# Kernel tuning notes

Hardware: AMD Instinct MI355X
Metric: run time of the kernel (lower is better)

The kernel has to match this reference:

```python
import jax, jax.numpy as jnp
import numpy as np

B, S, D, H = 2, 2048, 1024, 16
HD = D // H


def setup_inputs() -> dict:
    key = jax.random.key(0)
    ks = jax.random.split(key, 9)
    sc = 0.02
    return {
        "x": jax.random.normal(ks[0], (B, S, D), dtype=jnp.float32),
        "qw": jax.random.normal(ks[1], (D, D), dtype=jnp.float32) * sc,
        "qb": jax.random.normal(ks[2], (D,), dtype=jnp.float32) * sc,
        "kw": jax.random.normal(ks[3], (D, D), dtype=jnp.float32) * sc,
        "kb": jax.random.normal(ks[4], (D,), dtype=jnp.float32) * sc,
        "vw": jax.random.normal(ks[5], (D, D), dtype=jnp.float32) * sc,
        "vb": jax.random.normal(ks[6], (D,), dtype=jnp.float32) * sc,
        "ow": jax.random.normal(ks[7], (D, D), dtype=jnp.float32) * sc,
        "ob": jax.random.normal(ks[8], (D,), dtype=jnp.float32) * sc,
    }


def reference(x, qw, qb, kw, kb, vw, vb, ow, ob):
    b, s, d = x.shape
    # projections (torch Linear: x @ W.T + b)
    q = (x @ qw.T + qb).reshape(b, s, H, HD).transpose(0, 2, 1, 3)  # bhsd
    k = (x @ kw.T + kb).reshape(b, s, H, HD).transpose(0, 2, 1, 3)
    v = (x @ vw.T + vb).reshape(b, s, H, HD).transpose(0, 2, 1, 3)
    scale = 1.0 / jnp.sqrt(jnp.float32(HD))
    score = jnp.einsum("bhsd,bhtd->bhst", q, k) * scale  # bhss
    # causal mask: -inf strictly above diagonal
    mask = jnp.triu(jnp.full((s, s), -jnp.inf, dtype=score.dtype), k=1)
    score = jax.nn.softmax(score + mask, axis=-1)
    o = jnp.einsum("bhst,bhtd->bhsd", score, v)
    o = o.transpose(0, 2, 1, 3).reshape(b, s, d)
    return o @ ow.T + ob
```

## Files before the change

kernel.cpp:

```cpp
#include <hip/hip_runtime.h>
#include <hip/hip_bf16.h>
#include <stdint.h>

typedef __bf16 bf16x8 __attribute__((ext_vector_type(8)));
typedef __bf16 bf16x4 __attribute__((ext_vector_type(4)));
typedef float f32x4 __attribute__((ext_vector_type(4)));
typedef unsigned short ushort_t;


__device__ inline ushort_t f2bf(float f) {
  union { float f; uint32_t u; } v; v.f = f;
  uint32_t r = (v.u + 0x7fffu + ((v.u >> 16) & 1u)) >> 16;
  return (ushort_t)r;
}

__device__ inline void gll16(const void* g, void* l) {
  __builtin_amdgcn_global_load_lds((const __attribute__((address_space(1))) void*)g,
                                   (__attribute__((address_space(3))) void*)l, 16, 0, 0);
}

__global__ void cvt_x(const float* __restrict__ in, ushort_t* __restrict__ out) {
  int i = blockIdx.x * blockDim.x + threadIdx.x;
  float4 f = ((const float4*)in)[i];
  union { ushort_t u[4]; uint2 v; } r;
  r.u[0] = f2bf(f.x); r.u[1] = f2bf(f.y); r.u[2] = f2bf(f.z); r.u[3] = f2bf(f.w);
  ((uint2*)out)[i] = r.v;
}
__global__ void cvt_w(const float* __restrict__ a, const float* __restrict__ b,
                      const float* __restrict__ c, const float* __restrict__ d,
                      ushort_t* __restrict__ out) {
  const float* srcs[4] = {a, b, c, d};
  const float* s = srcs[blockIdx.y];
  ushort_t* o = out + (size_t)blockIdx.y * 1048576;
  int i = blockIdx.x * blockDim.x + threadIdx.x;
  float4 f = ((const float4*)s)[i];
  union { ushort_t u[4]; uint2 v; } r;
  r.u[0] = f2bf(f.x); r.u[1] = f2bf(f.y); r.u[2] = f2bf(f.z); r.u[3] = f2bf(f.w);
  ((uint2*)(o))[i] = r.v;
}

#define NKT 16

__device__ inline void stage_half(const ushort_t* __restrict__ g, ushort_t* l, int tid) {
  #pragma unroll
  for (int i = 0; i < 2; i++) {
    int c = tid + i * 512;
    int row = c >> 3;
    int q = (c & 7) ^ (row & 7);
    gll16(g + (size_t)row * 1024 + q * 8, l + c * 8);
  }
}

__global__ __launch_bounds__(512, 2) void qkv_gemm(
    const ushort_t* __restrict__ xb,
    const ushort_t* __restrict__ qwb, const ushort_t* __restrict__ kwb, const ushort_t* __restrict__ vwb,
    const float* __restrict__ qbias, const float* __restrict__ kbias, const float* __restrict__ vbias,
    ushort_t* __restrict__ qo, ushort_t* __restrict__ ko, ushort_t* __restrict__ vto)
{
  const int z = blockIdx.y;
  const int bx = blockIdx.x;
  const float* bias = (z == 0) ? qbias : (z == 1) ? kbias : vbias;
  const ushort_t* Ap;
  const ushort_t* Bp;
  int m0, n0;
  if (z == 2) {
    Ap = vwb; Bp = xb;
    m0 = (bx & 3) * 256;
    n0 = (bx >> 2) * 256;
  } else {
    Ap = xb; Bp = (z == 0) ? qwb : kwb;
    m0 = (bx >> 2) * 256;
    n0 = (bx & 3) * 256;
  }

  __shared__ __align__(16) ushort_t As[2][2][128 * 64];
  __shared__ __align__(16) ushort_t Bs[2][2][128 * 64];

  const int tid = threadIdx.x;
  const int w = tid >> 6;
  const int lane = tid & 63;
  const int ln = lane & 15;
  const int q4 = lane >> 4;
  const int wm = w & 1;
  const int wn = w >> 1;
  const int bh = wn >> 1;
  const int brow0 = (wn & 1) * 64;

  f32x4 acc[8][4];
  #pragma unroll
  for (int i = 0; i < 8; i++)
    #pragma unroll
    for (int j = 0; j < 4; j++) acc[i][j] = f32x4{0.f, 0.f, 0.f, 0.f};

  stage_half(Ap + (size_t)(m0 +   0) * 1024 +  0, &As[0][0][0], tid);
  stage_half(Ap + (size_t)(m0 + 128) * 1024 +  0, &As[0][1][0], tid);
  stage_half(Bp + (size_t)(n0 +   0) * 1024 +  0, &Bs[0][0][0], tid);
  stage_half(Bp + (size_t)(n0 + 128) * 1024 +  0, &Bs[0][1][0], tid);
  stage_half(Bp + (size_t)(n0 +   0) * 1024 + 64, &Bs[1][0][0], tid);
  stage_half(Bp + (size_t)(n0 + 128) * 1024 + 64, &Bs[1][1][0], tid);
  asm volatile("s_waitcnt vmcnt(4)" ::: "memory");
  __builtin_amdgcn_s_barrier();

  const int achk = ln & 7;

  for (int t = 0; t < NKT; ++t) {
    const int buf = t & 1;
    const ushort_t* Abuf = &As[buf][wm][0];
    const ushort_t* Bbuf = &Bs[buf][bh][0];

    bf16x8 a0[4][2], a4[4][2], b0[2][2], b2[2][2];

    #pragma unroll
    for (int m = 0; m < 4; m++)
      #pragma unroll
      for (int ks = 0; ks < 2; ks++)
        a0[m][ks] = *(const bf16x8*)&Abuf[(m * 16 + ln) * 64 + (((ks * 4 + q4) ^ achk) * 8)];
    #pragma unroll
    for (int n = 0; n < 2; n++)
      #pragma unroll
      for (int ks = 0; ks < 2; ks++)
        b0[n][ks] = *(const bf16x8*)&Bbuf[(brow0 + n * 16 + ln) * 64 + (((ks * 4 + q4) ^ achk) * 8)];
    if (t + 1 < NKT)
      stage_half(Ap + (size_t)m0 * 1024 + (t + 1) * 64, &As[(t + 1) & 1][0][0], tid);
    __builtin_amdgcn_s_barrier();
    asm volatile("s_waitcnt lgkmcnt(0)" ::: "memory");
    __builtin_amdgcn_s_setprio(1);
    #pragma unroll
    for (int m = 0; m < 4; m++)
      #pragma unroll
      for (int n = 0; n < 2; n++)
        #pragma unroll
        for (int ks = 0; ks < 2; ks++)
          acc[m][n] = __builtin_amdgcn_mfma_f32_16x16x32_bf16(a0[m][ks], b0[n][ks], acc[m][n], 0, 0, 0);
    __builtin_amdgcn_s_setprio(0);
    __builtin_amdgcn_s_barrier();

    #pragma unroll
    for (int n = 0; n < 2; n++)
      #pragma unroll
      for (int ks = 0; ks < 2; ks++)
        b2[n][ks] = *(const bf16x8*)&Bbuf[(brow0 + (n + 2) * 16 + ln) * 64 + (((ks * 4 + q4) ^ achk) * 8)];
    if (t + 1 < NKT)
      stage_half(Ap + (size_t)(m0 + 128) * 1024 + (t + 1) * 64, &As[(t + 1) & 1][1][0], tid);
    __builtin_amdgcn_s_barrier();
    asm volatile("s_waitcnt lgkmcnt(0)" ::: "memory");
    __builtin_amdgcn_s_setprio(1);
    #pragma unroll
    for (int m = 0; m < 4; m++)
      #pragma unroll
      for (int n = 0; n < 2; n++)
        #pragma unroll
        for (int ks = 0; ks < 2; ks++)
          acc[m][n + 2] = __builtin_amdgcn_mfma_f32_16x16x32_bf16(a0[m][ks], b2[n][ks], acc[m][n + 2], 0, 0, 0);
    __builtin_amdgcn_s_setprio(0);
    __builtin_amdgcn_s_barrier();

    #pragma unroll
    for (int m = 0; m < 4; m++)
      #pragma unroll
      for (int ks = 0; ks < 2; ks++)
        a4[m][ks] = *(const bf16x8*)&Abuf[((m + 4) * 16 + ln) * 64 + (((ks * 4 + q4) ^ achk) * 8)];
    if (t + 2 < NKT)
      stage_half(Bp + (size_t)n0 * 1024 + (t + 2) * 64, &Bs[buf][0][0], tid);
    __builtin_amdgcn_s_barrier();
    asm volatile("s_waitcnt lgkmcnt(0)" ::: "memory");
    __builtin_amdgcn_s_setprio(1);
    #pragma unroll
    for (int m = 0; m < 4; m++)
      #pragma unroll
      for (int n = 0; n < 2; n++)
        #pragma unroll
        for (int ks = 0; ks < 2; ks++)
          acc[m + 4][n + 2] = __builtin_amdgcn_mfma_f32_16x16x32_bf16(a4[m][ks], b2[n][ks], acc[m + 4][n + 2], 0, 0, 0);
    __builtin_amdgcn_s_setprio(0);
    __builtin_amdgcn_s_barrier();

    if (t + 2 < NKT)
      stage_half(Bp + (size_t)(n0 + 128) * 1024 + (t + 2) * 64, &Bs[buf][1][0], tid);
    __builtin_amdgcn_s_barrier();
    __builtin_amdgcn_s_setprio(1);
    #pragma unroll
    for (int m = 0; m < 4; m++)
      #pragma unroll
      for (int n = 0; n < 2; n++)
        #pragma unroll
        for (int ks = 0; ks < 2; ks++)
          acc[m + 4][n] = __builtin_amdgcn_mfma_f32_16x16x32_bf16(a4[m][ks], b0[n][ks], acc[m + 4][n], 0, 0, 0);
    __builtin_amdgcn_s_setprio(0);
    if (t + 2 < NKT) {
      asm volatile("s_waitcnt vmcnt(4)" ::: "memory");
    } else if (t + 1 < NKT) {
      asm volatile("s_waitcnt vmcnt(0)" ::: "memory");
    }
    __builtin_amdgcn_s_barrier();
  }

  if (z == 2) {
    #pragma unroll
    for (int n = 0; n < 4; n++) {
      int col = n0 + wn * 64 + n * 16 + ln;
      int bb = col >> 11, s = col & 2047;
      size_t base = (size_t)bb * 2097152 + s;
      #pragma unroll
      for (int m = 0; m < 8; m++) {
        int prow = m0 + wm * 128 + m * 16 + q4 * 4;
        #pragma unroll
        for (int r = 0; r < 4; r++) {
          int p = prow + r;
          vto[base + (size_t)p * 2048] = f2bf(acc[m][n][r] + bias[p]);
        }
      }
    }
  } else {
    #pragma unroll
    for (int n = 0; n < 4; n++) {
      int col = n0 + wn * 64 + n * 16 + ln;
      float bv = bias[col];
      int h = col >> 6, hd = col & 63;
      #pragma unroll
      for (int m = 0; m < 8; m++) {
        int rowb = m0 + wm * 128 + m * 16 + q4 * 4;
        #pragma unroll
        for (int r = 0; r < 4; r++) {
          int row = rowb + r;
          int b = row >> 11, s = row & 2047;
          float val = acc[m][n][r] + bv;
          if (z == 0) {
            qo[((size_t)((b * 16 + h) * 2048 + s)) * 64 + hd] = f2bf(val * 0.180336884f);
          } else {
            ko[((size_t)((b * 16 + h) * 2048 + s)) * 64 + hd] = f2bf(val);
          }
        }
      }
    }
  }
}

#define PAD 72
#define PPAD 68
__global__ __launch_bounds__(256) void attn(
    const ushort_t* __restrict__ qp, const ushort_t* __restrict__ kp,
    const ushort_t* __restrict__ vtp, ushort_t* __restrict__ op)
{
  __shared__ __align__(16) ushort_t Ks[64 * PAD];
  __shared__ __align__(16) ushort_t Vts[64 * PAD];
  __shared__ __align__(16) ushort_t Ps[4][16 * PPAD];

  const int tid = threadIdx.x;
  const int w = tid >> 6;
  const int lane = tid & 63;
  const int ln = lane & 15;
  const int q4 = lane >> 4;
  const int bh = blockIdx.y;
  const int b = bh >> 4, h = bh & 15;
  int tswz = (blockIdx.x + blockIdx.y) & 31;
  const int qt = (blockIdx.y & 16) ? (31 - tswz) : tswz;
  const int q0 = qt * 64;
  const int nt = qt + 1;

  const int c0 = tid, c1 = tid + 256;
  const int kr0_row = c0 >> 3, kr0_col = (c0 & 7) * 8;
  const int kr1_row = c1 >> 3, kr1_col = (c1 & 7) * 8;

  bf16x8 onesf;
  {
    union { ushort_t u[8]; bf16x8 v; } t;
    #pragma unroll
    for (int j = 0; j < 8; j++) t.u[j] = 0x3F80;
    onesf = t.v;
  }

  bf16x8 qf[2];
  {
    const ushort_t* base = qp + ((size_t)bh * 2048 + q0 + w * 16 + ln) * 64 + q4 * 8;
    qf[0] = *(const bf16x8*)(base);
    qf[1] = *(const bf16x8*)(base + 32);
  }

  f32x4 acc_o[4];
  f32x4 acc_l = f32x4{0.f, 0.f, 0.f, 0.f};
  #pragma unroll
  for (int t = 0; t < 4; t++) acc_o[t] = f32x4{0.f, 0.f, 0.f, 0.f};

  const ushort_t* kb = kp + (size_t)bh * 2048 * 64;
  const ushort_t* vb = vtp + (size_t)bh * 64 * 2048;

  uint4 kr0, kr1, vr0, vr1;
  kr0 = *(const uint4*)(kb + kr0_row * 64 + kr0_col);
  kr1 = *(const uint4*)(kb + kr1_row * 64 + kr1_col);
  vr0 = *(const uint4*)(vb + (size_t)kr0_row * 2048 + kr0_col);
  vr1 = *(const uint4*)(vb + (size_t)kr1_row * 2048 + kr1_col);

  for (int it = 0; it < nt; it++) {
    if (it) __syncthreads();
    *(uint4*)(&Ks [kr0_row * PAD + kr0_col]) = kr0;
    *(uint4*)(&Ks [kr1_row * PAD + kr1_col]) = kr1;
    *(uint4*)(&Vts[kr0_row * PAD + kr0_col]) = vr0;
    *(uint4*)(&Vts[kr1_row * PAD + kr1_col]) = vr1;
    __syncthreads();

    if (it + 1 < nt) {
      int kv1 = (it + 1) * 64;
      kr0 = *(const uint4*)(kb + (size_t)kv1 * 64 + kr0_row * 64 + kr0_col);
      kr1 = *(const uint4*)(kb + (size_t)kv1 * 64 + kr1_row * 64 + kr1_col);
      vr0 = *(const uint4*)(vb + (size_t)kr0_row * 2048 + kv1 + kr0_col);
      vr1 = *(const uint4*)(vb + (size_t)kr1_row * 2048 + kv1 + kr1_col);
    }

    f32x4 sc[4];
    #pragma unroll
    for (int t = 0; t < 4; t++) sc[t] = f32x4{0.f, 0.f, 0.f, 0.f};
    __builtin_amdgcn_s_setprio(1);
    #pragma unroll
    for (int ks = 0; ks < 2; ks++) {
      bf16x8 kf[4];
      #pragma unroll
      for (int tn = 0; tn < 4; tn++)
        kf[tn] = *(const bf16x8*)(&Ks[(tn * 16 + ln) * PAD + ks * 32 + q4 * 8]);
      #pragma unroll
      for (int tn = 0; tn < 4; tn++)
        sc[tn] = __builtin_amdgcn_mfma_f32_16x16x32_bf16(qf[ks], kf[tn], sc[tn], 0, 0, 0);
    }
    __builtin_amdgcn_s_setprio(0);

    if (it == qt) {
      int qrow = w * 16 + q4 * 4;
      #pragma unroll
      for (int tn = 0; tn < 4; tn++) {
        int col = tn * 16 + ln;
        #pragma unroll
        for (int r = 0; r < 4; r++)
          if (col > qrow + r) sc[tn][r] = -__builtin_inff();
      }
    }
    #pragma unroll
    for (int tn = 0; tn < 4; tn++)
      #pragma unroll
      for (int r = 0; r < 4; r++) {
        float p = __builtin_amdgcn_exp2f(sc[tn][r]);
        Ps[w][(q4 * 4 + r) * PPAD + tn * 16 + ln] = (ushort_t)(__float_as_uint(p) >> 16);
      }
    __builtin_amdgcn_s_setprio(1);
    #pragma unroll
    for (int ks = 0; ks < 2; ks++) {
      bf16x8 vf[4];
      #pragma unroll
      for (int tn = 0; tn < 4; tn++)
        vf[tn] = *(const bf16x8*)(&Vts[(tn * 16 + ln) * PAD + ks * 32 + q4 * 8]);
      const ushort_t* pp = &Ps[w][ln * PPAD + ks * 32 + q4 * 8];
      bf16x4 plo = *(const bf16x4*)(pp);
      bf16x4 phi = *(const bf16x4*)(pp + 4);
      bf16x8 pf = __builtin_shufflevector(plo, phi, 0, 1, 2, 3, 4, 5, 6, 7);
      acc_l = __builtin_amdgcn_mfma_f32_16x16x32_bf16(pf, onesf, acc_l, 0, 0, 0);
      #pragma unroll
      for (int tn = 0; tn < 4; tn++)
        acc_o[tn] = __builtin_amdgcn_mfma_f32_16x16x32_bf16(pf, vf[tn], acc_o[tn], 0, 0, 0);
    }
    __builtin_amdgcn_s_setprio(0);
  }

  {
    float invl[4];
    #pragma unroll
    for (int r = 0; r < 4; r++) invl[r] = __builtin_amdgcn_rcpf(acc_l[r]);
    #pragma unroll
    for (int tn = 0; tn < 4; tn++)
      #pragma unroll
      for (int r = 0; r < 4; r++) {
        int row = q0 + w * 16 + q4 * 4 + r;
        op[((size_t)b * 2048 + row) * 1024 + h * 64 + tn * 16 + ln] =
            f2bf(acc_o[tn][r] * invl[r]);
      }
  }
}

__global__ __launch_bounds__(256) void out_gemm(
    const ushort_t* __restrict__ ob_in, const ushort_t* __restrict__ owb,
    const float* __restrict__ obias, float* __restrict__ out)
{
  __shared__ __align__(16) ushort_t As[3][64 * 64];
  __shared__ __align__(16) ushort_t Bs[3][128 * 64];

  const int tid = threadIdx.x;
  const int w = tid >> 6;
  const int lane = tid & 63;
  const int ln = lane & 15;
  const int q4 = lane >> 4;
  const int wm = w & 1, wn = w >> 1;
  const int m0 = blockIdx.y * 64;
  const int n0 = blockIdx.x * 128;

  f32x4 acc[2][4];
  #pragma unroll
  for (int i = 0; i < 2; i++)
    #pragma unroll
    for (int j = 0; j < 4; j++) acc[i][j] = f32x4{0.f, 0.f, 0.f, 0.f};

  auto STAGE = [&](int bi, int k0) {
    #pragma unroll
    for (int i = 0; i < 2; i++) {
      int c = tid + i * 256;
      int row = c >> 3;
      int cq = (c & 7) ^ (row & 7);
      gll16(&ob_in[(size_t)(m0 + row) * 1024 + k0 + cq * 8], &As[bi][c * 8]);
    }
    #pragma unroll
    for (int i = 0; i < 4; i++) {
      int c = tid + i * 256;
      int row = c >> 3;
      int cq = (c & 7) ^ (row & 7);
      gll16(&owb[(size_t)(n0 + row) * 1024 + k0 + cq * 8], &Bs[bi][c * 8]);
    }
  };

  STAGE(0, 0);
  STAGE(1, 64);
  asm volatile("s_waitcnt vmcnt(6)" ::: "memory");
  __builtin_amdgcn_s_barrier();

  #pragma unroll
  for (int t = 0; t < 16; t++) {
    const int cb = t % 3;
    if (t + 2 < 16) STAGE((t + 2) % 3, (t + 2) * 64);
    #pragma unroll
    for (int ks = 0; ks < 2; ks++) {
      bf16x8 af[2], bfr[4];
      #pragma unroll
      for (int tt = 0; tt < 2; tt++) {
        int rr = wm * 32 + tt * 16 + ln;
        af[tt] = *(const bf16x8*)(&As[cb][rr * 64 + (((ks * 4 + q4) ^ (rr & 7)) * 8)]);
      }
      #pragma unroll
      for (int tt = 0; tt < 4; tt++) {
        int rc = wn * 64 + tt * 16 + ln;
        bfr[tt] = *(const bf16x8*)(&Bs[cb][rc * 64 + (((ks * 4 + q4) ^ (rc & 7)) * 8)]);
      }
      #pragma unroll
      for (int tm = 0; tm < 2; tm++)
        #pragma unroll
        for (int tn = 0; tn < 4; tn++)
          acc[tm][tn] = __builtin_amdgcn_mfma_f32_16x16x32_bf16(af[tm], bfr[tn], acc[tm][tn], 0, 0, 0);
    }
    if (t + 2 < 16) {
      asm volatile("s_waitcnt vmcnt(6)" ::: "memory");
    } else if (t + 1 < 16) {
      asm volatile("s_waitcnt vmcnt(0)" ::: "memory");
    }
    __builtin_amdgcn_s_barrier();
  }

  #pragma unroll
  for (int tn = 0; tn < 4; tn++) {
    int col = n0 + wn * 64 + tn * 16 + ln;
    float bv = obias[col];
    #pragma unroll
    for (int tm = 0; tm < 2; tm++) {
      int rowb = m0 + wm * 32 + tm * 16 + q4 * 4;
      #pragma unroll
      for (int r = 0; r < 4; r++)
        out[(size_t)(rowb + r) * 1024 + col] = acc[tm][tn][r] + bv;
    }
  }
}

extern "C" void kernel_launch(void* const* d_in, const int* in_sizes, int n_in,
                              void* d_out, int out_size, void* d_ws, size_t ws_size,
                              hipStream_t stream) {
  const float* x     = (const float*)d_in[0];
  const float* qw    = (const float*)d_in[1];
  const float* qb    = (const float*)d_in[2];
  const float* kw    = (const float*)d_in[3];
  const float* kb    = (const float*)d_in[4];
  const float* vw    = (const float*)d_in[5];
  const float* vb    = (const float*)d_in[6];
  const float* ow    = (const float*)d_in[7];
  const float* obias = (const float*)d_in[8];
  float* out = (float*)d_out;

  char* ws = (char*)d_ws;
  ushort_t* xb  = (ushort_t*)(ws);
  ushort_t* wb  = (ushort_t*)(ws + 8388608);
  ushort_t* qwb = wb;
  ushort_t* kwb = wb + 1048576;
  ushort_t* vwb = wb + 2097152;
  ushort_t* owb = wb + 3145728;
  ushort_t* qo  = (ushort_t*)(ws + 16777216);
  ushort_t* ko  = (ushort_t*)(ws + 25165824);
  ushort_t* vto = (ushort_t*)(ws + 33554432);
  ushort_t* oo  = (ushort_t*)(ws + 41943040);

  cvt_x<<<dim3(4096), dim3(256), 0, stream>>>(x, xb);
  cvt_w<<<dim3(1024, 4), dim3(256), 0, stream>>>(qw, kw, vw, ow, wb);

  qkv_gemm<<<dim3(64, 3), dim3(512), 0, stream>>>(xb, qwb, kwb, vwb, qb, kb, vb, qo, ko, vto);
  attn<<<dim3(32, 32), dim3(256), 0, stream>>>(qo, ko, vto, oo);
  out_gemm<<<dim3(8, 64), dim3(256), 0, stream>>>(oo, owb, obias, out);
}
```

Measured before the change: 193.5 us.

## Double-buffer attention K/V tiles with 128-row query blocks and merge conversion kernels

The attention kernel now processes 128 query rows per block with 8 waves, and K/V tiles are double-buffered in shared memory with loads issued two tiles ahead. This removes one of the two barriers per iteration and lets each K/V tile be reused by twice as many query rows. The x and weight fp32-to-bf16 conversions are merged into a single launch. The cost is more shared memory and registers per block, fewer blocks in the grid, and wasted fully-masked work on the last diagonal tile for the upper waves.

```diff
diff --git a/kernel.cpp b/kernel.cpp
--- a/kernel.cpp
+++ b/kernel.cpp
@@ -19,24 +19,28 @@
                                    (__attribute__((address_space(3))) void*)l, 16, 0, 0);
 }
 
-__global__ void cvt_x(const float* __restrict__ in, ushort_t* __restrict__ out) {
-  int i = blockIdx.x * blockDim.x + threadIdx.x;
-  float4 f = ((const float4*)in)[i];
-  union { ushort_t u[4]; uint2 v; } r;
-  r.u[0] = f2bf(f.x); r.u[1] = f2bf(f.y); r.u[2] = f2bf(f.z); r.u[3] = f2bf(f.w);
-  ((uint2*)out)[i] = r.v;
-}
-__global__ void cvt_w(const float* __restrict__ a, const float* __restrict__ b,
-                      const float* __restrict__ c, const float* __restrict__ d,
-                      ushort_t* __restrict__ out) {
-  const float* srcs[4] = {a, b, c, d};
-  const float* s = srcs[blockIdx.y];
-  ushort_t* o = out + (size_t)blockIdx.y * 1048576;
-  int i = blockIdx.x * blockDim.x + threadIdx.x;
+__global__ void cvt_all(const float* __restrict__ x,
+                        const float* __restrict__ qw, const float* __restrict__ kw,
+                        const float* __restrict__ vw, const float* __restrict__ ow,
+                        ushort_t* __restrict__ xb, ushort_t* __restrict__ wb) {
+  int bid = blockIdx.x;
+  const float* s;
+  ushort_t* o;
+  int i;
+  if (bid < 4096) {
+    s = x; o = xb; i = bid * 256 + threadIdx.x;
+  } else {
+    int j = bid - 4096;
+    int wi = j >> 10;
+    const float* srcs[4] = {qw, kw, vw, ow};
+    s = srcs[wi];
+    o = wb + (size_t)wi * 1048576;
+    i = (j & 1023) * 256 + threadIdx.x;
+  }
   float4 f = ((const float4*)s)[i];
   union { ushort_t u[4]; uint2 v; } r;
   r.u[0] = f2bf(f.x); r.u[1] = f2bf(f.y); r.u[2] = f2bf(f.z); r.u[3] = f2bf(f.w);
-  ((uint2*)(o))[i] = r.v;
+  ((uint2*)o)[i] = r.v;
 }
 
 #define NKT 16
@@ -238,13 +242,13 @@
 
 #define PAD 72
 #define PPAD 68
-__global__ __launch_bounds__(256) void attn(
+__global__ __launch_bounds__(512) void attn(
     const ushort_t* __restrict__ qp, const ushort_t* __restrict__ kp,
     const ushort_t* __restrict__ vtp, ushort_t* __restrict__ op)
 {
-  __shared__ __align__(16) ushort_t Ks[64 * PAD];
-  __shared__ __align__(16) ushort_t Vts[64 * PAD];
-  __shared__ __align__(16) ushort_t Ps[4][16 * PPAD];
+  __shared__ __align__(16) ushort_t Ks[2][64 * PAD];
+  __shared__ __align__(16) ushort_t Vts[2][64 * PAD];
+  __shared__ __align__(16) ushort_t Ps[8][16 * PPAD];
 
   const int tid = threadIdx.x;
   const int w = tid >> 6;
@@ -253,14 +257,12 @@
   const int q4 = lane >> 4;
   const int bh = blockIdx.y;
   const int b = bh >> 4, h = bh & 15;
-  int tswz = (blockIdx.x + blockIdx.y) & 31;
-  const int qt = (blockIdx.y & 16) ? (31 - tswz) : tswz;
-  const int q0 = qt * 64;
-  const int nt = qt + 1;
-
-  const int c0 = tid, c1 = tid + 256;
-  const int kr0_row = c0 >> 3, kr0_col = (c0 & 7) * 8;
-  const int kr1_row = c1 >> 3, kr1_col = (c1 & 7) * 8;
+  int tswz = (blockIdx.x + blockIdx.y) & 15;
+  const int qt = (blockIdx.y & 16) ? (15 - tswz) : tswz;
+  const int q0 = qt * 128;
+  const int nt = 2 * qt + 2;
+
+  const int kr_row = tid >> 3, kr_col = (tid & 7) * 8;
 
   bf16x8 onesf;
   {
@@ -285,26 +287,26 @@
   const ushort_t* kb = kp + (size_t)bh * 2048 * 64;
   const ushort_t* vb = vtp + (size_t)bh * 64 * 2048;
 
-  uint4 kr0, kr1, vr0, vr1;
-  kr0 = *(const uint4*)(kb + kr0_row * 64 + kr0_col);
-  kr1 = *(const uint4*)(kb + kr1_row * 64 + kr1_col);
-  vr0 = *(const uint4*)(vb + (size_t)kr0_row * 2048 + kr0_col);
-  vr1 = *(const uint4*)(vb + (size_t)kr1_row * 2048 + kr1_col);
+  uint4 kr, vr;
+  kr = *(const uint4*)(kb + kr_row * 64 + kr_col);
+  vr = *(const uint4*)(vb + (size_t)kr_row * 2048 + kr_col);
+  *(uint4*)(&Ks [0][kr_row * PAD + kr_col]) = kr;
+  *(uint4*)(&Vts[0][kr_row * PAD + kr_col]) = vr;
+  kr = *(const uint4*)(kb + 64 * 64 + kr_row * 64 + kr_col);
+  vr = *(const uint4*)(vb + (size_t)kr_row * 2048 + 64 + kr_col);
 
   for (int it = 0; it < nt; it++) {
-    if (it) __syncthreads();
-    *(uint4*)(&Ks [kr0_row * PAD + kr0_col]) = kr0;
-    *(uint4*)(&Ks [kr1_row * PAD + kr1_col]) = kr1;
-    *(uint4*)(&Vts[kr0_row * PAD + kr0_col]) = vr0;
-    *(uint4*)(&Vts[kr1_row * PAD + kr1_col]) = vr1;
+    const int cur = it & 1;
     __syncthreads();
-
     if (it + 1 < nt) {
-      int kv1 = (it + 1) * 64;
-      kr0 = *(const uint4*)(kb + (size_t)kv1 * 64 + kr0_row * 64 + kr0_col);
-      kr1 = *(const uint4*)(kb + (size_t)kv1 * 64 + kr1_row * 64 + kr1_col);
-      vr0 = *(const uint4*)(vb + (size_t)kr0_row * 2048 + kv1 + kr0_col);
-      vr1 = *(const uint4*)(vb + (size_t)kr1_row * 2048 + kv1 + kr1_col);
+      const int nxt = cur ^ 1;
+      *(uint4*)(&Ks [nxt][kr_row * PAD + kr_col]) = kr;
+      *(uint4*)(&Vts[nxt][kr_row * PAD + kr_col]) = vr;
+    }
+    if (it + 2 < nt) {
+      int kv2 = (it + 2) * 64;
+      kr = *(const uint4*)(kb + (size_t)kv2 * 64 + kr_row * 64 + kr_col);
+      vr = *(const uint4*)(vb + (size_t)kr_row * 2048 + kv2 + kr_col);
     }
 
     f32x4 sc[4];
@@ -316,18 +318,19 @@
       bf16x8 kf[4];
       #pragma unroll
       for (int tn = 0; tn < 4; tn++)
-        kf[tn] = *(const bf16x8*)(&Ks[(tn * 16 + ln) * PAD + ks * 32 + q4 * 8]);
+        kf[tn] = *(const bf16x8*)(&Ks[cur][(tn * 16 + ln) * PAD + ks * 32 + q4 * 8]);
       #pragma unroll
       for (int tn = 0; tn < 4; tn++)
         sc[tn] = __builtin_amdgcn_mfma_f32_16x16x32_bf16(qf[ks], kf[tn], sc[tn], 0, 0, 0);
     }
     __builtin_amdgcn_s_setprio(0);
 
-    if (it == qt) {
-      int qrow = w * 16 + q4 * 4;
+    if (it >= 2 * qt) {
+      int qrow = q0 + w * 16 + q4 * 4;
+      int kv0 = it * 64;
       #pragma unroll
       for (int tn = 0; tn < 4; tn++) {
-        int col = tn * 16 + ln;
+        int col = kv0 + tn * 16 + ln;
         #pragma unroll
         for (int r = 0; r < 4; r++)
           if (col > qrow + r) sc[tn][r] = -__builtin_inff();
@@ -346,7 +349,7 @@
       bf16x8 vf[4];
       #pragma unroll
       for (int tn = 0; tn < 4; tn++)
-        vf[tn] = *(const bf16x8*)(&Vts[(tn * 16 + ln) * PAD + ks * 32 + q4 * 8]);
+        vf[tn] = *(const bf16x8*)(&Vts[cur][(tn * 16 + ln) * PAD + ks * 32 + q4 * 8]);
       const ushort_t* pp = &Ps[w][ln * PPAD + ks * 32 + q4 * 8];
       bf16x4 plo = *(const bf16x4*)(pp);
       bf16x4 phi = *(const bf16x4*)(pp + 4);
@@ -489,10 +492,9 @@
   ushort_t* vto = (ushort_t*)(ws + 33554432);
   ushort_t* oo  = (ushort_t*)(ws + 41943040);
 
-  cvt_x<<<dim3(4096), dim3(256), 0, stream>>>(x, xb);
-  cvt_w<<<dim3(1024, 4), dim3(256), 0, stream>>>(qw, kw, vw, ow, wb);
+  cvt_all<<<dim3(8192), dim3(256), 0, stream>>>(x, qw, kw, vw, ow, xb, wb);
 
   qkv_gemm<<<dim3(64, 3), dim3(512), 0, stream>>>(xb, qwb, kwb, vwb, qb, kb, vb, qo, ko, vto);
-  attn<<<dim3(32, 32), dim3(256), 0, stream>>>(qo, ko, vto, oo);
+  attn<<<dim3(16, 32), dim3(512), 0, stream>>>(qo, ko, vto, oo);
   out_gemm<<<dim3(8, 64), dim3(256), 0, stream>>>(oo, owb, obias, out);
 }
```

After: 180.5 us. 1.07x faster.
